# Kernel tuning notes

Hardware: AMD Instinct MI355X
Metric: run time of the kernel (lower is better)

Reference implementation:

```python
import jax, jax.numpy as jnp
import numpy as np

D_MODEL = 1024
NUM_HEADS = 16
H_DIM = 4096
EPS = 1e-5


def setup_inputs() -> dict:
    key = jax.random.key(0)
    ks = jax.random.split(key, 16)
    B, S, D, H = 2, 2048, D_MODEL, H_DIM
    s = 0.02
    return {
        "x": jax.random.normal(ks[0], (B, S, D), jnp.float32),
        "wq": jax.random.normal(ks[1], (D, D), jnp.float32) * s,
        "bq": jnp.zeros((D,), jnp.float32),
        "wk": jax.random.normal(ks[2], (D, D), jnp.float32) * s,
        "bk": jnp.zeros((D,), jnp.float32),
        "wv": jax.random.normal(ks[3], (D, D), jnp.float32) * s,
        "bv": jnp.zeros((D,), jnp.float32),
        "wo": jax.random.normal(ks[4], (D, D), jnp.float32) * s,
        "bo": jnp.zeros((D,), jnp.float32),
        "ln1_g": jnp.ones((D,), jnp.float32),
        "ln1_b": jnp.zeros((D,), jnp.float32),
        "w1": jax.random.normal(ks[5], (H, D), jnp.float32) * s,
        "b1": jnp.zeros((H,), jnp.float32),
        "w2": jax.random.normal(ks[6], (D, H), jnp.float32) * s,
        "b2": jnp.zeros((D,), jnp.float32),
        "ln2_g": jnp.ones((D,), jnp.float32),
        "ln2_b": jnp.zeros((D,), jnp.float32),
    }


def _layer_norm(x, g, b):
    mu = jnp.mean(x, axis=-1, keepdims=True)
    var = jnp.mean(jnp.square(x - mu), axis=-1, keepdims=True)
    return (x - mu) * jax.lax.rsqrt(var + EPS) * g + b


def _mhsa(x, wq, bq, wk, bk, wv, bv, wo, bo):
    B, S, D = x.shape
    Hh, hd = NUM_HEADS, D // NUM_HEADS
    q = (x @ wq.T + bq).reshape(B, S, Hh, hd)
    k = (x @ wk.T + bk).reshape(B, S, Hh, hd)
    v = (x @ wv.T + bv).reshape(B, S, Hh, hd)
    scale = hd ** -0.5
    scores = jnp.einsum('bqhd,bkhd->bhqk', q, k) * scale
    att = jax.nn.softmax(scores, axis=-1)
    out = jnp.einsum('bhqk,bkhd->bqhd', att, v).reshape(B, S, D)
    return out @ wo.T + bo


def reference(x, wq, bq, wk, bk, wv, bv, wo, bo, ln1_g, ln1_b,
              w1, b1, w2, b2, ln2_g, ln2_b):
    # pre-norm variant as written in the torch source:
    # x = norm1(x); x = x + msa(x)  (residual uses NORMALIZED x)
    x = _layer_norm(x, ln1_g, ln1_b)
    x = x + _mhsa(x, wq, bq, wk, bk, wv, bv, wo, bo)
    x = _layer_norm(x, ln2_g, ln2_b)
    h = jax.nn.gelu(x @ w1.T + b1, approximate=False)
    x = x + (h @ w2.T + b2)
    return x
```

## Files before the change

### kernel.cpp

```cpp
#include <hip/hip_runtime.h>
#include <hip/hip_bf16.h>

typedef unsigned short u16;
typedef __attribute__((ext_vector_type(8))) short short8;
typedef __attribute__((ext_vector_type(4))) float f32x4;

#define DM 1024
#define HM 4096
#define NHEADS 16
#define HD 64
#define SQ 2048
#define NBATCH 2
#define NTOK 4096

#define NX  ((size_t)NTOK * DM)

__device__ __forceinline__ u16 f2b(float f) {
    union { float f; unsigned int i; } w; w.f = f;
    unsigned int x = w.i;
    return (u16)((x + 0x7FFFu + ((x >> 16) & 1u)) >> 16);
}

__device__ __forceinline__ void gload_lds16(const void* g, void* l) {
    __builtin_amdgcn_global_load_lds(
        (const __attribute__((address_space(1))) void*)g,
        (__attribute__((address_space(3))) void*)l, 16, 0, 0);
}

__global__ void cvt_all(const float* __restrict__ wq, const float* __restrict__ wk,
                        const float* __restrict__ wv, const float* __restrict__ wo,
                        const float* __restrict__ w1, const float* __restrict__ w2,
                        const float* __restrict__ bq, const float* __restrict__ bk,
                        const float* __restrict__ bv, float* __restrict__ bias_dst,
                        u16* __restrict__ dst) {
    const int NW4 = DM * DM / 4;
    int i = blockIdx.x * 256 + threadIdx.x;
    if (i < 12 * NW4) {
        const float* src; int base; float sc = 1.0f;
        if      (i <     NW4) { src = wq; base = 0;       sc = 0.125f; }
        else if (i < 2 * NW4) { src = wk; base = NW4; }
        else if (i < 3 * NW4) { src = wv; base = 2 * NW4; }
        else if (i < 4 * NW4) { src = wo; base = 3 * NW4; }
        else if (i < 8 * NW4) { src = w1; base = 4 * NW4; }
        else                  { src = w2; base = 8 * NW4; }
        float4 f = ((const float4*)src)[i - base];
        ushort4 o;
        o.x = f2b(f.x * sc); o.y = f2b(f.y * sc);
        o.z = f2b(f.z * sc); o.w = f2b(f.w * sc);
        ((ushort4*)dst)[i] = o;
    } else {
        int j = i - 12 * NW4;
        if (j < 3 * DM) {
            float v = (j < DM) ? bq[j] * 0.125f
                    : (j < 2 * DM) ? bk[j - DM] : bv[j - 2 * DM];
            bias_dst[j] = v;
        }
    }
}

__global__ void ln_kernel(const float* __restrict__ xin, const float* __restrict__ g,
                          const float* __restrict__ b, float* __restrict__ outf,
                          u16* __restrict__ outb) {
    int t = blockIdx.x, tid = threadIdx.x;
    float4 f = ((const float4*)(xin + (size_t)t * DM))[tid];
    float v0 = f.x, v1 = f.y, v2 = f.z, v3 = f.w;
    float s  = v0 + v1 + v2 + v3;
    float ss = v0*v0 + v1*v1 + v2*v2 + v3*v3;
    #pragma unroll
    for (int o = 32; o > 0; o >>= 1) {
        s  += __shfl_down(s,  o, 64);
        ss += __shfl_down(ss, o, 64);
    }
    __shared__ float rs[4], rss[4];
    int w = tid >> 6, lane = tid & 63;
    if (!lane) { rs[w] = s; rss[w] = ss; }
    __syncthreads();
    s  = rs[0] + rs[1] + rs[2] + rs[3];
    ss = rss[0] + rss[1] + rss[2] + rss[3];
    float mean = s * (1.0f / DM);
    float var  = ss * (1.0f / DM) - mean * mean;
    float rstd = rsqrtf(var + 1e-5f);
    float4 gu = ((const float4*)g)[tid];
    float4 bu = ((const float4*)b)[tid];
    float4 o;
    o.x = (v0 - mean) * rstd * gu.x + bu.x;
    o.y = (v1 - mean) * rstd * gu.y + bu.y;
    o.z = (v2 - mean) * rstd * gu.z + bu.z;
    o.w = (v3 - mean) * rstd * gu.w + bu.w;
    ((float4*)(outf + (size_t)t * DM))[tid] = o;
    ushort4 ob; ob.x = f2b(o.x); ob.y = f2b(o.y); ob.z = f2b(o.z); ob.w = f2b(o.w);
    ((ushort4*)(outb + (size_t)t * DM))[tid] = ob;
}

__global__ void vtr_kernel(const u16* __restrict__ qkv, u16* __restrict__ vT) {
    __shared__ u16 tile[64][72];
    int bid = blockIdx.x;
    int tt = bid & 31, bh = bid >> 5;
    int h = bh & (NHEADS - 1), b = bh >> 4;
    int tid = threadIdx.x;
    int r = tid >> 2, c0 = (tid & 3) << 4;
    const u16* src = qkv + ((size_t)(b * SQ + tt * 64 + r)) * (3 * DM) + 2 * DM + h * HD + c0;
    #pragma unroll
    for (int j = 0; j < 4; j++)
        *(ushort4*)&tile[r][c0 + (j << 2)] = *(const ushort4*)(src + (j << 2));
    __syncthreads();
    int dd = tid >> 2, t0 = (tid & 3) << 4;
    u16* dst = vT + ((size_t)bh * HD + dd) * SQ + tt * 64 + t0;
    #pragma unroll
    for (int j = 0; j < 4; j++) {
        ushort4 v;
        v.x = tile[t0 + (j << 2) + 0][dd];
        v.y = tile[t0 + (j << 2) + 1][dd];
        v.z = tile[t0 + (j << 2) + 2][dd];
        v.w = tile[t0 + (j << 2) + 3][dd];
        *(ushort4*)(dst + (j << 2)) = v;
    }
}

template<int GELU, int RESID, int OUTBF>
__global__ __launch_bounds__(256, 2)
void gemm_bt(const u16* __restrict__ A, const u16* __restrict__ W,
             const float* __restrict__ bias, const float* __restrict__ resid,
             void* __restrict__ Cout, int M, int N, int K) {
    __shared__ __attribute__((aligned(16))) u16 As[2 * 128 * 64];
    __shared__ __attribute__((aligned(16))) u16 Bs[2 * 128 * 64];
    int tid  = threadIdx.x;
    int wid  = tid >> 6, lane = tid & 63;
    int m0 = blockIdx.y << 7, n0 = blockIdx.x << 7;
    int wm = (wid & 1) << 6, wn = (wid >> 1) << 6;

    int rIn = lane >> 3;
    int cSw = (((lane & 7) ^ (lane >> 3)) << 3);
    int s0  = wid << 2;
    int fr = lane & 15;
    int ksw0 = (((lane >> 4) ^ (lane & 7)) << 3);
    int ksw1 = (((4 + (lane >> 4)) ^ (lane & 7)) << 3);

    f32x4 acc[4][4];
    #pragma unroll
    for (int i = 0; i < 4; i++)
        #pragma unroll
        for (int j = 0; j < 4; j++)
            acc[i][j] = (f32x4){0.f, 0.f, 0.f, 0.f};

    #pragma unroll
    for (int t = 0; t < 4; t++) {
        int s = s0 + t;
        gload_lds16(A + (size_t)(m0 + (s << 3) + rIn) * K + cSw, As + (s << 9));
        gload_lds16(W + (size_t)(n0 + (s << 3) + rIn) * K + cSw, Bs + (s << 9));
    }
    __syncthreads();

    int nk = K >> 6;
    for (int kt = 0; kt < nk; kt++) {
        int buf = kt & 1;
        const u16* Ab = As + (buf << 13);
        const u16* Bb = Bs + (buf << 13);
        if (kt + 1 < nk) {
            int k0 = (kt + 1) << 6;
            int bo = (buf ^ 1) << 13;
            #pragma unroll
            for (int t = 0; t < 4; t++) {
                int s = s0 + t;
                gload_lds16(A + (size_t)(m0 + (s << 3) + rIn) * K + k0 + cSw, As + bo + (s << 9));
                gload_lds16(W + (size_t)(n0 + (s << 3) + rIn) * K + k0 + cSw, Bs + bo + (s << 9));
            }
        }
        #pragma unroll
        for (int ch = 0; ch < 2; ch++) {
            int ks = ch ? ksw1 : ksw0;
            short8 af[4], bf[4];
            #pragma unroll
            for (int mi = 0; mi < 4; mi++)
                af[mi] = *(const short8*)(Ab + (size_t)(wm + (mi << 4) + fr) * 64 + ks);
            #pragma unroll
            for (int ni = 0; ni < 4; ni++)
                bf[ni] = *(const short8*)(Bb + (size_t)(wn + (ni << 4) + fr) * 64 + ks);
            #pragma unroll
            for (int mi = 0; mi < 4; mi++)
                #pragma unroll
                for (int ni = 0; ni < 4; ni++)
                    acc[mi][ni] = __builtin_amdgcn_mfma_f32_16x16x32_bf16(
                        af[mi], bf[ni], acc[mi][ni], 0, 0, 0);
        }
        __syncthreads();
    }

    int erow = (lane >> 4) << 2;
    #pragma unroll
    for (int ni = 0; ni < 4; ni++) {
        int col = n0 + wn + (ni << 4) + fr;
        float bv = bias[col];
        #pragma unroll
        for (int mi = 0; mi < 4; mi++) {
            #pragma unroll
            for (int r = 0; r < 4; r++) {
                int row = m0 + wm + (mi << 4) + erow + r;
                float val = acc[mi][ni][r] + bv;
                if (GELU)  val = 0.5f * val * (1.0f + erff(val * 0.70710678118654752f));
                if (RESID) val += resid[(size_t)row * N + col];
                if (OUTBF) ((u16*)Cout)[(size_t)row * N + col] = f2b(val);
                else       ((float*)Cout)[(size_t)row * N + col] = val;
            }
        }
    }
}

template<int GELU, int RESID, int OUTBF>
__global__ __launch_bounds__(256, 3)
void gemm_n64(const u16* __restrict__ A, const u16* __restrict__ W,
              const float* __restrict__ bias, const float* __restrict__ resid,
              void* __restrict__ Cout, int M, int N, int K) {
    __shared__ __attribute__((aligned(16))) u16 As[2 * 128 * 64];
    __shared__ __attribute__((aligned(16))) u16 Bs[2 * 64 * 64];
    int tid  = threadIdx.x;
    int wid  = tid >> 6, lane = tid & 63;
    int nwgx = gridDim.x;
    int bidl = blockIdx.y * nwgx + blockIdx.x;
    int cpx  = (nwgx * gridDim.y) >> 3;
    int swz  = (bidl & 7) * cpx + (bidl >> 3);
    int m0 = (swz / nwgx) << 7, n0 = (swz % nwgx) << 6;
    int wm = (wid & 1) << 6, wn = (wid >> 1) << 5;

    int rIn = lane >> 3;
    int cSw = (((lane & 7) ^ (lane >> 3)) << 3);
    int sA = wid << 2;
    int sB = wid << 1;
    int fr = lane & 15;
    int ksw0 = (((lane >> 4) ^ (lane & 7)) << 3);
    int ksw1 = (((4 + (lane >> 4)) ^ (lane & 7)) << 3);

    f32x4 acc[4][2];
    #pragma unroll
    for (int i = 0; i < 4; i++)
        #pragma unroll
        for (int j = 0; j < 2; j++)
            acc[i][j] = (f32x4){0.f, 0.f, 0.f, 0.f};

    #pragma unroll
    for (int t = 0; t < 4; t++) {
        int s = sA + t;
        gload_lds16(A + (size_t)(m0 + (s << 3) + rIn) * K + cSw, As + (s << 9));
    }
    #pragma unroll
    for (int t = 0; t < 2; t++) {
        int s = sB + t;
        gload_lds16(W + (size_t)(n0 + (s << 3) + rIn) * K + cSw, Bs + (s << 9));
    }
    __syncthreads();

    int nk = K >> 6;
    for (int kt = 0; kt < nk; kt++) {
        int buf = kt & 1;
        const u16* Ab = As + (buf << 13);
        const u16* Bb = Bs + (buf << 12);
        if (kt + 1 < nk) {
            int k0 = (kt + 1) << 6;
            int boA = (buf ^ 1) << 13;
            int boB = (buf ^ 1) << 12;
            #pragma unroll
            for (int t = 0; t < 4; t++) {
                int s = sA + t;
                gload_lds16(A + (size_t)(m0 + (s << 3) + rIn) * K + k0 + cSw, As + boA + (s << 9));
            }
            #pragma unroll
            for (int t = 0; t < 2; t++) {
                int s = sB + t;
                gload_lds16(W + (size_t)(n0 + (s << 3) + rIn) * K + k0 + cSw, Bs + boB + (s << 9));
            }
        }
        #pragma unroll
        for (int ch = 0; ch < 2; ch++) {
            int ks = ch ? ksw1 : ksw0;
            short8 af[4], bf[2];
            #pragma unroll
            for (int mi = 0; mi < 4; mi++)
                af[mi] = *(const short8*)(Ab + (size_t)(wm + (mi << 4) + fr) * 64 + ks);
            #pragma unroll
            for (int ni = 0; ni < 2; ni++)
                bf[ni] = *(const short8*)(Bb + (size_t)(wn + (ni << 4) + fr) * 64 + ks);
            #pragma unroll
            for (int mi = 0; mi < 4; mi++)
                #pragma unroll
                for (int ni = 0; ni < 2; ni++)
                    acc[mi][ni] = __builtin_amdgcn_mfma_f32_16x16x32_bf16(
                        af[mi], bf[ni], acc[mi][ni], 0, 0, 0);
        }
        __syncthreads();
    }

    int erow = (lane >> 4) << 2;
    #pragma unroll
    for (int ni = 0; ni < 2; ni++) {
        int col = n0 + wn + (ni << 4) + fr;
        float bv = bias[col];
        #pragma unroll
        for (int mi = 0; mi < 4; mi++) {
            #pragma unroll
            for (int r = 0; r < 4; r++) {
                int row = m0 + wm + (mi << 4) + erow + r;
                float val = acc[mi][ni][r] + bv;
                if (GELU)  val = 0.5f * val * (1.0f + erff(val * 0.70710678118654752f));
                if (RESID) val += resid[(size_t)row * N + col];
                if (OUTBF) ((u16*)Cout)[(size_t)row * N + col] = f2b(val);
                else       ((float*)Cout)[(size_t)row * N + col] = val;
            }
        }
    }
}

__global__ __launch_bounds__(256) void fattn_mfma(const u16* __restrict__ QKV,
                                                  const u16* __restrict__ VT,
                                                  u16* __restrict__ O) {
    __shared__ __attribute__((aligned(16))) u16 QP[4096];
    __shared__ __attribute__((aligned(16))) u16 Ks[2][4096];
    __shared__ __attribute__((aligned(16))) u16 Vt[2][4096];
    const int ld = 3 * DM;
    int bid = ((blockIdx.x & 7) << 7) + (blockIdx.x >> 3);
    int qt = bid & 31, bh = bid >> 5;
    int h = bh & (NHEADS - 1), b = bh >> 4;
    int tid = threadIdx.x, wid = tid >> 6, lane = tid & 63;
    int fr = lane & 15;
    int fcs = (((lane >> 4) ^ ((fr >> 1) & 3)) << 3);
    int lsw = (((lane & 3) ^ ((lane >> 3) & 3)) << 3);
    size_t tokb = (size_t)b * SQ;
    const u16* Qg  = QKV + tokb * ld + h * HD;
    const u16* Kg  = QKV + tokb * ld + DM + h * HD;
    const u16* VTg = VT + ((size_t)bh * HD) * SQ;
    int s0 = wid << 1;

    {
        #pragma unroll
        for (int t = 0; t < 2; t++) {
            int s = s0 + t;
            const u16* g = Qg + (size_t)(qt * 64 + ((s & 3) << 4) + (lane >> 2)) * ld
                         + ((s >> 2) << 5) + lsw;
            gload_lds16(g, QP + (s << 9));
        }
    }
    {
        #pragma unroll
        for (int t = 0; t < 2; t++) {
            int s = s0 + t;
            const u16* g = Kg + (size_t)(((s & 3) << 4) + (lane >> 2)) * ld
                         + ((s >> 2) << 5) + lsw;
            gload_lds16(g, Ks[0] + (s << 9));
            const u16* gv = VTg + (size_t)(((s & 3) << 4) + (lane >> 2)) * SQ
                          + ((s >> 2) << 5) + lsw;
            gload_lds16(gv, Vt[0] + (s << 9));
        }
    }
    f32x4 oacc[4];
    #pragma unroll
    for (int di = 0; di < 4; di++) oacc[di] = (f32x4){0.f, 0.f, 0.f, 0.f};
    float lsum = 0.f;
    __syncthreads();
    short8 aq0 = *(const short8*)(QP + ((wid << 4) + fr) * 32 + fcs);
    short8 aq1 = *(const short8*)(QP + 2048 + ((wid << 4) + fr) * 32 + fcs);

    for (int kt = 0; kt < SQ / 64; kt++) {
        int buf = kt & 1;
        if (kt + 1 < SQ / 64) {
            #pragma unroll
            for (int t = 0; t < 2; t++) {
                int s = s0 + t;
                const u16* g = Kg + (size_t)((kt + 1) * 64 + ((s & 3) << 4) + (lane >> 2)) * ld
                             + ((s >> 2) << 5) + lsw;
                gload_lds16(g, Ks[buf ^ 1] + (s << 9));
                const u16* gv = VTg + (size_t)(((s & 3) << 4) + (lane >> 2)) * SQ
                              + (kt + 1) * 64 + ((s >> 2) << 5) + lsw;
                gload_lds16(gv, Vt[buf ^ 1] + (s << 9));
            }
        }
        float p[4][4];
        #pragma unroll
        for (int ni = 0; ni < 4; ni++) {
            short8 bk0 = *(const short8*)(Ks[buf] + ((ni << 4) + fr) * 32 + fcs);
            short8 bk1 = *(const short8*)(Ks[buf] + 2048 + ((ni << 4) + fr) * 32 + fcs);
            f32x4 z = (f32x4){0.f, 0.f, 0.f, 0.f};
            __builtin_amdgcn_s_setprio(1);
            z = __builtin_amdgcn_mfma_f32_16x16x32_bf16(bk0, aq0, z, 0, 0, 0);
            z = __builtin_amdgcn_mfma_f32_16x16x32_bf16(bk1, aq1, z, 0, 0, 0);
            __builtin_amdgcn_s_setprio(0);
            #pragma unroll
            for (int r = 0; r < 4; r++) {
                float e = __expf(z[r]);
                lsum += e;
                p[ni][r] = e;
            }
        }
        unsigned int W[4][2];
        #pragma unroll
        for (int ni = 0; ni < 4; ni++) {
            asm("v_cvt_pk_bf16_f32 %0, %1, %2" : "=v"(W[ni][0]) : "v"(p[ni][0]), "v"(p[ni][1]));
            asm("v_cvt_pk_bf16_f32 %0, %1, %2" : "=v"(W[ni][1]) : "v"(p[ni][2]), "v"(p[ni][3]));
        }
        union { unsigned int w[4]; short8 v; } fA0, fA1;
        #pragma unroll
        for (int w = 0; w < 2; w++) {
            unsigned int a0 = W[0][w], b0 = W[1][w];
            asm("v_permlane32_swap_b32 %0, %1" : "+v"(a0), "+v"(b0));
            asm("v_permlane16_swap_b32 %0, %1" : "+v"(a0), "+v"(b0));
            fA0.w[w] = a0; fA0.w[w + 2] = b0;
            unsigned int a1 = W[2][w], b1 = W[3][w];
            asm("v_permlane32_swap_b32 %0, %1" : "+v"(a1), "+v"(b1));
            asm("v_permlane16_swap_b32 %0, %1" : "+v"(a1), "+v"(b1));
            fA1.w[w] = a1; fA1.w[w + 2] = b1;
        }
        short8 ap0 = fA0.v, ap1 = fA1.v;
        __builtin_amdgcn_s_setprio(1);
        #pragma unroll
        for (int di = 0; di < 4; di++) {
            short8 bv0 = *(const short8*)(Vt[buf] + ((di << 4) + fr) * 32 + fcs);
            short8 bv1 = *(const short8*)(Vt[buf] + 2048 + ((di << 4) + fr) * 32 + fcs);
            oacc[di] = __builtin_amdgcn_mfma_f32_16x16x32_bf16(ap0, bv0, oacc[di], 0, 0, 0);
            oacc[di] = __builtin_amdgcn_mfma_f32_16x16x32_bf16(ap1, bv1, oacc[di], 0, 0, 0);
        }
        __builtin_amdgcn_s_setprio(0);
        __syncthreads();
    }
    lsum += __shfl_xor(lsum, 16, 64);
    lsum += __shfl_xor(lsum, 32, 64);
    float inv = 1.0f / lsum;
    float invq[4];
    #pragma unroll
    for (int r = 0; r < 4; r++)
        invq[r] = __shfl(inv, ((lane >> 4) << 2) + r, 64);
    #pragma unroll
    for (int di = 0; di < 4; di++) {
        int d = (di << 4) + fr;
        #pragma unroll
        for (int r = 0; r < 4; r++) {
            int q = qt * 64 + (wid << 4) + ((lane >> 4) << 2) + r;
            O[(tokb + q) * DM + h * HD + d] = f2b(oacc[di][r] * invq[r]);
        }
    }
}

extern "C" void kernel_launch(void* const* d_in, const int* in_sizes, int n_in,
                              void* d_out, int out_size, void* d_ws, size_t ws_size,
                              hipStream_t stream) {
    if (n_in < 17) return;
    const float* x   = (const float*)d_in[0];
    const float* wq  = (const float*)d_in[1];
    const float* bq  = (const float*)d_in[2];
    const float* wk  = (const float*)d_in[3];
    const float* bk  = (const float*)d_in[4];
    const float* wv  = (const float*)d_in[5];
    const float* bv  = (const float*)d_in[6];
    const float* wo  = (const float*)d_in[7];
    const float* bo  = (const float*)d_in[8];
    const float* g1  = (const float*)d_in[9];
    const float* e1  = (const float*)d_in[10];
    const float* w1  = (const float*)d_in[11];
    const float* b1  = (const float*)d_in[12];
    const float* w2  = (const float*)d_in[13];
    const float* b2  = (const float*)d_in[14];
    const float* g2  = (const float*)d_in[15];
    const float* e2  = (const float*)d_in[16];

    float* F = (float*)d_ws;
    size_t off = 0;
    float* xnf   = F + off; off += NX;
    u16*   xnb   = (u16*)(F + off); off += NX / 2;
    u16*   qkvb  = (u16*)(F + off); off += (size_t)NTOK * 3 * DM / 2;
    u16*   vTb   = (u16*)(F + off); off += (size_t)NTOK * DM / 2;
    float* y     = F + off; off += NX;
    u16*   aob   = (u16*)(F + off); off += NX / 2;
    u16*   hb    = (u16*)(F + off); off += (size_t)NTOK * HM / 2;
    u16*   wqkvb = (u16*)(F + off); off += (size_t)3 * DM * DM / 2;
    u16*   wob   = (u16*)(F + off); off += (size_t)DM * DM / 2;
    u16*   w1b   = (u16*)(F + off); off += (size_t)HM * DM / 2;
    u16*   w2b   = (u16*)(F + off); off += (size_t)DM * HM / 2;
    float* bqkv  = F + off; off += 3 * DM;
    if (ws_size < off * sizeof(float)) return;

    dim3 blk(256);
    cvt_all<<<(12 * DM * DM / 4 + 3 * DM + 255) / 256, blk, 0, stream>>>(
        wq, wk, wv, wo, w1, w2, bq, bk, bv, bqkv, wqkvb);

    ln_kernel<<<NTOK, blk, 0, stream>>>(x, g1, e1, xnf, xnb);
    gemm_bt<0,0,1><<<dim3(3 * DM / 128, NTOK / 128), blk, 0, stream>>>(
        xnb, wqkvb, bqkv, nullptr, qkvb, NTOK, 3 * DM, DM);
    vtr_kernel<<<NBATCH * NHEADS * (SQ / 64), blk, 0, stream>>>(qkvb, vTb);
    fattn_mfma<<<NBATCH * NHEADS * (SQ / 64), blk, 0, stream>>>(qkvb, vTb, aob);
    gemm_n64<0,1,0><<<dim3(DM / 64, NTOK / 128), blk, 0, stream>>>(
        aob, wob, bo, xnf, y, NTOK, DM, DM);
    ln_kernel<<<NTOK, blk, 0, stream>>>(y, g2, e2, xnf, xnb);
    gemm_bt<1,0,1><<<dim3(HM / 128, NTOK / 128), blk, 0, stream>>>(
        xnb, w1b, b1, nullptr, hb, NTOK, HM, DM);
    gemm_n64<0,1,0><<<dim3(DM / 64, NTOK / 128), blk, 0, stream>>>(
        hb, w2b, b2, xnf, d_out, NTOK, DM, HM);
}
```

Before: 375.0 us.

## Use 4-stage K=32 LDS pipeline with explicit vmcnt waits in GEMM

Replaces the double-buffered K=64 tile loop in the bf16 GEMM with a 4-slot ring of K=32 half-tiles, prefetching three stages ahead. Each iteration waits with s_waitcnt vmcnt and a single barrier instead of two syncthreads per step. The aim is to hide global load latency better and cut barrier overhead, with a new swizzle for the 32-wide rows. The risk is more iterations with fewer MFMAs between barriers, and hand-counted vmcnt values that assume the compiler emits no other loads.

```diff
diff --git a/kernel.cpp b/kernel.cpp
--- a/kernel.cpp
+++ b/kernel.cpp
@@ -122,19 +122,17 @@
 void gemm_bt(const u16* __restrict__ A, const u16* __restrict__ W,
              const float* __restrict__ bias, const float* __restrict__ resid,
              void* __restrict__ Cout, int M, int N, int K) {
-    __shared__ __attribute__((aligned(16))) u16 As[2 * 128 * 64];
-    __shared__ __attribute__((aligned(16))) u16 Bs[2 * 128 * 64];
+    __shared__ __attribute__((aligned(16))) u16 As[4 * 128 * 32];
+    __shared__ __attribute__((aligned(16))) u16 Bs[4 * 128 * 32];
     int tid  = threadIdx.x;
     int wid  = tid >> 6, lane = tid & 63;
     int m0 = blockIdx.y << 7, n0 = blockIdx.x << 7;
     int wm = (wid & 1) << 6, wn = (wid >> 1) << 6;
 
-    int rIn = lane >> 3;
-    int cSw = (((lane & 7) ^ (lane >> 3)) << 3);
-    int s0  = wid << 2;
-    int fr = lane & 15;
-    int ksw0 = (((lane >> 4) ^ (lane & 7)) << 3);
-    int ksw1 = (((4 + (lane >> 4)) ^ (lane & 7)) << 3);
+    int fr  = lane & 15;
+    int fcs = (((lane >> 4) ^ ((fr >> 1) & 3)) << 3);
+    int lsw = (((lane & 3) ^ ((lane >> 3) & 3)) << 3);
+    int rStg = lane >> 2;
 
     f32x4 acc[4][4];
     #pragma unroll
@@ -143,47 +141,52 @@
         for (int j = 0; j < 4; j++)
             acc[i][j] = (f32x4){0.f, 0.f, 0.f, 0.f};
 
-    #pragma unroll
-    for (int t = 0; t < 4; t++) {
-        int s = s0 + t;
-        gload_lds16(A + (size_t)(m0 + (s << 3) + rIn) * K + cSw, As + (s << 9));
-        gload_lds16(W + (size_t)(n0 + (s << 3) + rIn) * K + cSw, Bs + (s << 9));
-    }
-    __syncthreads();
-
-    int nk = K >> 6;
-    for (int kt = 0; kt < nk; kt++) {
-        int buf = kt & 1;
-        const u16* Ab = As + (buf << 13);
-        const u16* Bb = Bs + (buf << 13);
-        if (kt + 1 < nk) {
-            int k0 = (kt + 1) << 6;
-            int bo = (buf ^ 1) << 13;
-            #pragma unroll
-            for (int t = 0; t < 4; t++) {
-                int s = s0 + t;
-                gload_lds16(A + (size_t)(m0 + (s << 3) + rIn) * K + k0 + cSw, As + bo + (s << 9));
-                gload_lds16(W + (size_t)(n0 + (s << 3) + rIn) * K + k0 + cSw, Bs + bo + (s << 9));
-            }
-        }
-        #pragma unroll
-        for (int ch = 0; ch < 2; ch++) {
-            int ks = ch ? ksw1 : ksw0;
-            short8 af[4], bf[4];
-            #pragma unroll
-            for (int mi = 0; mi < 4; mi++)
-                af[mi] = *(const short8*)(Ab + (size_t)(wm + (mi << 4) + fr) * 64 + ks);
+    const int NHP = K >> 5;
+
+    for (int hp = 0; hp < 3; hp++) {
+        int k0 = hp << 5, so = (hp & 3) << 12;
+        #pragma unroll
+        for (int t = 0; t < 2; t++) {
+            int seg = (wid << 1) + t;
+            int row = (seg << 4) + rStg;
+            gload_lds16(A + (size_t)(m0 + row) * K + k0 + lsw, As + so + (seg << 9));
+            gload_lds16(W + (size_t)(n0 + row) * K + k0 + lsw, Bs + so + (seg << 9));
+        }
+    }
+
+    for (int hp = 0; hp < NHP; hp++) {
+        if (hp + 3 <= NHP) {
+            asm volatile("s_waitcnt vmcnt(8)" ::: "memory");
+        } else if (hp + 2 == NHP) {
+            asm volatile("s_waitcnt vmcnt(4)" ::: "memory");
+        } else {
+            asm volatile("s_waitcnt vmcnt(0)" ::: "memory");
+        }
+        __builtin_amdgcn_s_barrier();
+        if (hp + 3 < NHP) {
+            int k0 = (hp + 3) << 5, so = ((hp + 3) & 3) << 12;
+            #pragma unroll
+            for (int t = 0; t < 2; t++) {
+                int seg = (wid << 1) + t;
+                int row = (seg << 4) + rStg;
+                gload_lds16(A + (size_t)(m0 + row) * K + k0 + lsw, As + so + (seg << 9));
+                gload_lds16(W + (size_t)(n0 + row) * K + k0 + lsw, Bs + so + (seg << 9));
+            }
+        }
+        int so = (hp & 3) << 12;
+        short8 af[4], bf[4];
+        #pragma unroll
+        for (int mi = 0; mi < 4; mi++)
+            af[mi] = *(const short8*)(As + so + (wm + (mi << 4) + fr) * 32 + fcs);
+        #pragma unroll
+        for (int ni = 0; ni < 4; ni++)
+            bf[ni] = *(const short8*)(Bs + so + (wn + (ni << 4) + fr) * 32 + fcs);
+        #pragma unroll
+        for (int mi = 0; mi < 4; mi++)
             #pragma unroll
             for (int ni = 0; ni < 4; ni++)
-                bf[ni] = *(const short8*)(Bb + (size_t)(wn + (ni << 4) + fr) * 64 + ks);
-            #pragma unroll
-            for (int mi = 0; mi < 4; mi++)
-                #pragma unroll
-                for (int ni = 0; ni < 4; ni++)
-                    acc[mi][ni] = __builtin_amdgcn_mfma_f32_16x16x32_bf16(
-                        af[mi], bf[ni], acc[mi][ni], 0, 0, 0);
-        }
-        __syncthreads();
+                acc[mi][ni] = __builtin_amdgcn_mfma_f32_16x16x32_bf16(
+                    af[mi], bf[ni], acc[mi][ni], 0, 0, 0);
     }
 
     int erow = (lane >> 4) << 2;
```

Result: slower. 391.5 us (+4.4%).
